# Kernel tuning notes

Hardware: AMD Instinct MI355X
Metric: run time of the kernel (lower is better)

Reference implementation:

```python
import jax, jax.numpy as jnp
import numpy as np

B, S, F_IN = 64, 168, 10
D, H, L = 512, 8, 4
HID, F_OUT, N_FUT = 2048, 1, 48
EPS = 1e-9


def _pos_encoding(d, position=168):
    pos = np.arange(position)[:, None].astype(np.float32)
    i = np.arange(d)[None, :].astype(np.float32)
    angle = pos / np.power(10000.0, 2.0 * (np.floor(i / 2.0)) / np.float32(d))
    angle[:, 0::2] = np.sin(angle[:, 0::2])
    angle[:, 1::2] = np.cos(angle[:, 1::2])
    return jnp.asarray(angle[None, ...], dtype=jnp.float32)  # [1, position, d]


def setup_inputs() -> dict:
    key = jax.random.key(0)
    ks = iter(jax.random.split(key, 64))
    s = 0.02

    def w(shape):
        return (jax.random.normal(next(ks), shape, jnp.float32) * s)

    inp = {
        "x": jax.random.normal(next(ks), (B, S, F_IN), jnp.float32),
        "mask": jnp.triu(jnp.ones((S, S), jnp.float32), k=1)[None, None],  # [1,1,S,S]
        "in_w": w((F_IN, D)), "in_b": jnp.zeros((D,), jnp.float32),
        "wq_w": w((L, D, D * H)), "wq_b": jnp.zeros((L, D * H), jnp.float32),
        "wk_w": w((L, D, D * H)), "wk_b": jnp.zeros((L, D * H), jnp.float32),
        "wv_w": w((L, D, D * H)), "wv_b": jnp.zeros((L, D * H), jnp.float32),
        "dn_w": w((L, D * H, D)), "dn_b": jnp.zeros((L, D), jnp.float32),
        "mh_w": w((L, D, HID)), "mh_b": jnp.zeros((L, HID), jnp.float32),
        "mo_w": w((L, HID, D)), "mo_b": jnp.zeros((L, D), jnp.float32),
        "ln1_g": jnp.ones((L, D), jnp.float32), "ln1_b": jnp.zeros((L, D), jnp.float32),
        "ln3_g": jnp.ones((L, D), jnp.float32), "ln3_b": jnp.zeros((L, D), jnp.float32),
        "out_w": w((D, F_OUT)), "out_b": jnp.zeros((F_OUT,), jnp.float32),
    }
    return inp


def _ln(h, g, b):
    m = jnp.mean(h, axis=-1, keepdims=True)
    v = jnp.mean((h - m) ** 2, axis=-1, keepdims=True)
    return (h - m) * jax.lax.rsqrt(v + EPS) * g + b


def _split(t):  # [B,S,H*D] -> [B,H,S,D]
    return t.reshape(B, S, H, D).transpose(0, 2, 1, 3)


def reference(x, mask, in_w, in_b, wq_w, wq_b, wk_w, wk_b, wv_w, wv_b,
              dn_w, dn_b, mh_w, mh_b, mo_w, mo_b,
              ln1_g, ln1_b, ln3_g, ln3_b, out_w, out_b):
    pe = _pos_encoding(D)  # [1,168,D]
    h = x @ in_w + in_b
    h = h * jnp.sqrt(jnp.float32(D)) + pe[:, :S, :]
    inv_sqrt_d = 1.0 / jnp.sqrt(jnp.float32(D))
    for i in range(L):
        q = _split(h @ wq_w[i] + wq_b[i])
        k = _split(h @ wk_w[i] + wk_b[i])
        v = _split(h @ wv_w[i] + wv_b[i])
        scores = jnp.einsum('bhqd,bhkd->bhqk', q, k) * inv_sqrt_d
        scores = scores + mask * (-1e9)
        attn_w = jax.nn.softmax(scores, axis=-1)
        att = jnp.einsum('bhqk,bhkd->bhqd', attn_w, v)
        att = att.transpose(0, 2, 1, 3).reshape(B, S, H * D)
        att = att @ dn_w[i] + dn_b[i]
        h1 = _ln(att + h, ln1_g[i], ln1_b[i])
        mlp = jax.nn.relu(h1 @ mh_w[i] + mh_b[i]) @ mo_w[i] + mo_b[i]
        h = _ln(mlp + h1, ln3_g[i], ln3_b[i])
    out = h @ out_w + out_b
    return out[:, -N_FUT:, :]
```

## Files before the change

### kernel.cpp

```cpp
#include <hip/hip_runtime.h>
#include <hip/hip_bf16.h>

typedef __bf16 bf16;
typedef __bf16 bf16x8 __attribute__((ext_vector_type(8)));
typedef float f32x4 __attribute__((ext_vector_type(4)));

#define MODE_BIAS 1
#define MODE_RELU 2
#define MODE_BF16 4
#define MODE_F32  8
#define MODE_RES  16
#define MODE_RESB 32
#define MODE_QKV  128

__device__ __forceinline__ void stage16(const bf16* g, bf16* l)
{
  __builtin_amdgcn_global_load_lds(
      (const __attribute__((address_space(1))) void*)g,
      (__attribute__((address_space(3))) void*)l, 16, 0, 0);
}

__global__ __launch_bounds__(256) void gemm2(
    const bf16* __restrict__ A, const bf16* __restrict__ B,
    float* __restrict__ Cf, bf16* __restrict__ Cb,
    const float* __restrict__ bias, const float* __restrict__ resf,
    const bf16* __restrict__ resb,
    int N, int K, int lda, int ldb, int ldc, long qstride, int mode)
{
  __shared__ __attribute__((aligned(16))) bf16 smem[24576];
  bf16* sA = smem;
  bf16* sB = smem + 12288;

  int tid  = threadIdx.x;
  int lane = tid & 63;
  int wave = tid >> 6;
  int wm = (wave >> 1) * 64;
  int wn = (wave & 1) * 64;

  int nwg = gridDim.x * gridDim.y;
  int i0  = blockIdx.y * gridDim.x + blockIdx.x;
  int q   = nwg >> 3, r = nwg & 7;
  int xcd = i0 & 7, jj = i0 >> 3;
  int lid = (xcd < r ? xcd * (q + 1) : r * (q + 1) + (xcd - r) * q) + jj;
  int bx = lid % gridDim.x;
  int by = lid / gridDim.x;
  int bm0 = bx * 128;
  int bn0 = by * 128;

  f32x4 acc[4][4];
  #pragma unroll
  for (int i = 0; i < 4; ++i)
    #pragma unroll
    for (int j = 0; j < 4; ++j)
      #pragma unroll
      for (int rr = 0; rr < 4; ++rr) acc[i][j][rr] = 0.f;

  int seg0 = wave, seg1 = wave + 4;
  int csw = ((lane & 3) ^ ((lane >> 3) & 3)) * 16;
  int r0s = seg0 * 16 + (lane >> 2);
  int r1s = seg1 * 16 + (lane >> 2);
  int rx = ((lane >> 4) ^ ((lane >> 1) & 3)) * 8;

  const char* gA0 = (const char*)A + ((long)(bm0 + r0s) * lda) * 2 + csw;
  const char* gA1 = (const char*)A + ((long)(bm0 + r1s) * lda) * 2 + csw;
  const char* gB0 = (const char*)B + ((long)(bn0 + r0s) * ldb) * 2 + csw;
  const char* gB1 = (const char*)B + ((long)(bn0 + r1s) * ldb) * 2 + csw;

  int nt = K >> 5;

  stage16((const bf16*)gA0, sA + seg0 * 512);
  stage16((const bf16*)gA1, sA + seg1 * 512);
  stage16((const bf16*)gB0, sB + seg0 * 512);
  stage16((const bf16*)gB1, sB + seg1 * 512);
  stage16((const bf16*)(gA0 + 64), sA + 4096 + seg0 * 512);
  stage16((const bf16*)(gA1 + 64), sA + 4096 + seg1 * 512);
  stage16((const bf16*)(gB0 + 64), sB + 4096 + seg0 * 512);
  stage16((const bf16*)(gB1 + 64), sB + 4096 + seg1 * 512);

  int slot = 0, sslot = 2;
  for (int t = 0; t < nt; ++t) {
    if (t + 2 < nt) {
      long ob = (long)(t + 2) * 64;
      int so = sslot * 4096;
      stage16((const bf16*)(gA0 + ob), sA + so + seg0 * 512);
      stage16((const bf16*)(gA1 + ob), sA + so + seg1 * 512);
      stage16((const bf16*)(gB0 + ob), sB + so + seg0 * 512);
      stage16((const bf16*)(gB1 + ob), sB + so + seg1 * 512);
      asm volatile("s_waitcnt vmcnt(8)" ::: "memory");
    } else if (t + 1 < nt) {
      asm volatile("s_waitcnt vmcnt(4)" ::: "memory");
    } else {
      asm volatile("s_waitcnt vmcnt(0)" ::: "memory");
    }
    asm volatile("s_barrier" ::: "memory");
    __builtin_amdgcn_sched_barrier(0);
    int po = slot * 4096;
    bf16x8 aF[4], bF[4];
    #pragma unroll
    for (int i = 0; i < 4; ++i)
      aF[i] = *(const bf16x8*)(&sA[po + (wm + i * 16 + (lane & 15)) * 32 + rx]);
    #pragma unroll
    for (int j = 0; j < 4; ++j)
      bF[j] = *(const bf16x8*)(&sB[po + (wn + j * 16 + (lane & 15)) * 32 + rx]);
    __builtin_amdgcn_s_setprio(1);
    #pragma unroll
    for (int i = 0; i < 4; ++i)
      #pragma unroll
      for (int j = 0; j < 4; ++j)
        acc[i][j] = __builtin_amdgcn_mfma_f32_16x16x32_bf16(aF[i], bF[j], acc[i][j], 0, 0, 0);
    __builtin_amdgcn_s_setprio(0);
    asm volatile("s_waitcnt lgkmcnt(0)" ::: "memory");
    __builtin_amdgcn_sched_barrier(0);
    asm volatile("s_barrier" ::: "memory");
    slot = (slot == 2) ? 0 : slot + 1;
    sslot = (sslot == 2) ? 0 : sslot + 1;
  }

  int lg = lane >> 4;
  int r0 = lg * 4;
  int cc = lane & 15;

  if ((mode & MODE_QKV) && bn0 >= 8192) {
    bf16* sS = smem;
    int nn0 = bn0 - 8192;
    #pragma unroll
    for (int ph = 0; ph < 2; ++ph) {
      if ((wn >> 6) == ph) {
        #pragma unroll
        for (int j = 0; j < 4; ++j) {
          int nl = j * 16 + cc;
          float bv = bias[bn0 + wn + j * 16 + cc];
          #pragma unroll
          for (int i = 0; i < 4; ++i)
            #pragma unroll
            for (int rr = 0; rr < 4; ++rr) {
              int m = wm + i * 16 + r0 + rr;
              sS[nl * 130 + m] = (bf16)(acc[i][j][rr] + bv);
            }
        }
      }
      __syncthreads();
      #pragma unroll
      for (int u = 0; u < 16; ++u) {
        int nrow = u * 4 + wave;
        int d = nn0 + ph * 64 + nrow;
        int hh = d >> 9, dd = d & 511;
        unsigned int pv = *(const unsigned int*)&sS[nrow * 130 + lane * 2];
        int m0 = bm0 + 2 * lane;
        int bl = m0 / 168;
        int s  = m0 - bl * 168;
        *(unsigned int*)&Cb[2 * qstride + ((long)(bl * 8 + hh) * 512 + dd) * 168 + s] = pv;
      }
      __syncthreads();
    }
    return;
  }

  if (mode & (MODE_QKV | MODE_BF16)) {
    bf16* sS = smem;
    #pragma unroll
    for (int j = 0; j < 4; ++j) {
      float bv = (mode & MODE_BIAS) ? bias[bn0 + wn + j * 16 + cc] : 0.f;
      #pragma unroll
      for (int i = 0; i < 4; ++i) {
        #pragma unroll
        for (int rr = 0; rr < 4; ++rr) {
          float v = acc[i][j][rr] + bv;
          if (mode & MODE_RELU) v = fmaxf(v, 0.f);
          sS[(wm + i * 16 + r0 + rr) * 136 + wn + j * 16 + cc] = (bf16)v;
        }
      }
    }
    __syncthreads();
    long base;
    int ldx;
    if (mode & MODE_QKV) {
      int part = bn0 >> 12;
      base = (long)part * qstride + (bn0 & 4095);
      ldx = 4096;
    } else {
      base = (long)bn0;
      ldx = ldc;
    }
    #pragma unroll
    for (int it = 0; it < 8; ++it) {
      int idx = it * 256 + tid;
      int row = idx >> 4, seg = idx & 15;
      bf16x8 v = *(const bf16x8*)&sS[row * 136 + seg * 8];
      *(bf16x8*)&Cb[base + (long)(bm0 + row) * ldx + seg * 8] = v;
    }
    return;
  }

  #pragma unroll
  for (int j = 0; j < 4; ++j) {
    int gn = bn0 + wn + j * 16 + cc;
    float bv = (mode & MODE_BIAS) ? bias[gn] : 0.f;
    #pragma unroll
    for (int i = 0; i < 4; ++i) {
      #pragma unroll
      for (int rr = 0; rr < 4; ++rr) {
        int gm = bm0 + wm + i * 16 + r0 + rr;
        float v = acc[i][j][rr] + bv;
        if (mode & MODE_RES)  v += resf[(long)gm * ldc + gn];
        if (mode & MODE_RESB) v += (float)resb[(long)gm * ldc + gn];
        if (mode & MODE_RELU) v = fmaxf(v, 0.f);
        if (mode & MODE_F32) {
          Cf[(long)gm * ldc + gn] = v;
        } else {
          Cb[(long)gm * ldc + gn] = (bf16)v;
        }
      }
    }
  }
}

__global__ __launch_bounds__(256) void attn_fused(
    const bf16* __restrict__ Q, const bf16* __restrict__ K,
    const bf16* __restrict__ Vt, bf16* __restrict__ O)
{
  __shared__ __attribute__((aligned(16))) bf16 sQ[2 * 64 * 32];
  __shared__ __attribute__((aligned(16))) bf16 sK[2 * 192 * 32];
  __shared__ __attribute__((aligned(16))) bf16 sP[64 * 200];
  __shared__ __attribute__((aligned(16))) bf16 sV[256 * 32];

  int mt = blockIdx.x;
  int bh = blockIdx.y;
  int bl = bh >> 3, h = bh & 7;
  int tid = threadIdx.x, lane = tid & 63, wave = tid >> 6;

  const bf16* Qb = Q + ((long)bl * 168 + mt * 64) * 4096 + h * 512;
  const bf16* Kb = K + (long)bl * 168 * 4096 + h * 512;
  const bf16* Vb = Vt + (long)bh * 512 * 168;

  #pragma unroll
  for (int idx = tid; idx < 64 * 16; idx += 256) {
    int rr = idx >> 4;
    sP[rr * 200 + 176 + (idx & 15)] = (bf16)0.f;
  }

  int srw = wave * 16 + (lane >> 2);
  int scb = ((lane & 3) ^ ((lane >> 3) & 3)) * 16;
  int rx  = ((lane >> 4) ^ ((lane >> 1) & 3)) * 8;

  const char* gQ = (const char*)Qb + (long)srw * 8192 + scb;
  const char* gK = (const char*)Kb + (long)srw * 8192 + scb;

  f32x4 sacc[11];
  #pragma unroll
  for (int j = 0; j < 11; ++j)
    #pragma unroll
    for (int rr = 0; rr < 4; ++rr) sacc[j][rr] = 0.f;

  stage16((const bf16*)gQ, &sQ[wave * 512]);
  stage16((const bf16*)gK, &sK[wave * 512]);
  stage16((const bf16*)(gK + 64 * 8192), &sK[(wave + 4) * 512]);
  stage16((const bf16*)(gK + 128 * 8192), &sK[(wave + 8) * 512]);

  for (int t = 0; t < 16; ++t) {
    int p = t & 1;
    if (t < 15) {
      long ob = (long)(t + 1) * 64;
      int bq = (p ^ 1) * 2048, bk = (p ^ 1) * 6144;
      stage16((const bf16*)(gQ + ob), &sQ[bq + wave * 512]);
      stage16((const bf16*)(gK + ob), &sK[bk + wave * 512]);
      stage16((const bf16*)(gK + 64 * 8192 + ob), &sK[bk + (wave + 4) * 512]);
      stage16((const bf16*)(gK + 128 * 8192 + ob), &sK[bk + (wave + 8) * 512]);
      asm volatile("s_waitcnt vmcnt(4)" ::: "memory");
    } else {
      asm volatile("s_waitcnt vmcnt(0)" ::: "memory");
    }
    asm volatile("s_barrier" ::: "memory");
    __builtin_amdgcn_sched_barrier(0);
    bf16x8 aF = *(const bf16x8*)(&sQ[p * 2048 + (wave * 16 + (lane & 15)) * 32 + rx]);
    __builtin_amdgcn_s_setprio(1);
    #pragma unroll
    for (int j = 0; j < 11; ++j) {
      bf16x8 bF = *(const bf16x8*)(&sK[p * 6144 + (j * 16 + (lane & 15)) * 32 + rx]);
      sacc[j] = __builtin_amdgcn_mfma_f32_16x16x32_bf16(aF, bF, sacc[j], 0, 0, 0);
    }
    __builtin_amdgcn_s_setprio(0);
    asm volatile("s_waitcnt lgkmcnt(0)" ::: "memory");
    __builtin_amdgcn_sched_barrier(0);
    asm volatile("s_barrier" ::: "memory");
  }

  int rbase = wave * 16 + ((lane >> 4) << 2);
  #pragma unroll
  for (int rr = 0; rr < 4; ++rr) {
    int srow = mt * 64 + rbase + rr;
    float mx = -1e30f;
    #pragma unroll
    for (int j = 0; j < 11; ++j) {
      int col = j * 16 + (lane & 15);
      float v = sacc[j][rr] * 0.04419417382415922f;
      v = (col <= srow) ? v : -1e9f;
      sacc[j][rr] = v;
      mx = fmaxf(mx, v);
    }
    #pragma unroll
    for (int off = 1; off < 16; off <<= 1) mx = fmaxf(mx, __shfl_xor(mx, off, 16));
    float sum = 0.f;
    #pragma unroll
    for (int j = 0; j < 11; ++j) {
      float e = __expf(sacc[j][rr] - mx);
      sacc[j][rr] = e;
      sum += e;
    }
    #pragma unroll
    for (int off = 1; off < 16; off <<= 1) sum += __shfl_xor(sum, off, 16);
    float inv = 1.f / sum;
    #pragma unroll
    for (int j = 0; j < 11; ++j)
      sP[(rbase + rr) * 200 + j * 16 + (lane & 15)] = (bf16)(sacc[j][rr] * inv);
  }

  const char* gV = (const char*)Vb + (long)srw * 336 + scb;
  #pragma unroll 1
  for (int nc = 0; nc < 2; ++nc) {
    f32x4 oacc[16];
    #pragma unroll
    for (int t = 0; t < 16; ++t)
      #pragma unroll
      for (int rr = 0; rr < 4; ++rr) oacc[t][rr] = 0.f;

    for (int k0 = 0; k0 < 192; k0 += 32) {
      #pragma unroll
      for (int u = 0; u < 4; ++u)
        stage16((const bf16*)(gV + (long)(nc * 256 + u * 64) * 336 + (long)k0 * 2),
                &sV[(wave + u * 4) * 512]);
      __syncthreads();
      bf16x8 aF = *(const bf16x8*)(&sP[(wave * 16 + (lane & 15)) * 200 + k0 + (lane >> 4) * 8]);
      __builtin_amdgcn_s_setprio(1);
      #pragma unroll
      for (int t = 0; t < 16; ++t) {
        bf16x8 bF = *(const bf16x8*)(&sV[(t * 16 + (lane & 15)) * 32 + rx]);
        oacc[t] = __builtin_amdgcn_mfma_f32_16x16x32_bf16(aF, bF, oacc[t], 0, 0, 0);
      }
      __builtin_amdgcn_s_setprio(0);
      __syncthreads();
    }
    #pragma unroll
    for (int t = 0; t < 16; ++t) {
      int d = nc * 256 + t * 16 + (lane & 15);
      #pragma unroll
      for (int rr = 0; rr < 4; ++rr) {
        int srow = mt * 64 + rbase + rr;
        if (srow < 168)
          O[((long)bl * 168 + srow) * 4096 + h * 512 + d] = (bf16)oacc[t][rr];
      }
    }
  }
}

__global__ __launch_bounds__(256) void transpose_w(const float* __restrict__ in,
                                                   bf16* __restrict__ out,
                                                   int K, int N, long ostride, long obase)
{
  long zi = (long)blockIdx.z * K * N;
  long zo = (long)blockIdx.z * ostride + obase;
  __shared__ float t[32][33];
  int tx = threadIdx.x & 31;
  int ty = threadIdx.x >> 5;
  int n0 = blockIdx.x * 32;
  int k0 = blockIdx.y * 32;
  #pragma unroll
  for (int r = 0; r < 4; ++r) {
    int k = k0 + ty + r * 8, n = n0 + tx;
    if (k < K && n < N) t[ty + r * 8][tx] = in[zi + (long)k * N + n];
  }
  __syncthreads();
  #pragma unroll
  for (int r = 0; r < 4; ++r) {
    int n = n0 + ty + r * 8, k = k0 + tx;
    if (n < N && k < K) out[zo + (long)n * K + k] = (bf16)t[tx][ty + r * 8];
  }
}

__global__ __launch_bounds__(256) void merge_bias(const float* __restrict__ q,
                                                  const float* __restrict__ k,
                                                  const float* __restrict__ v,
                                                  float* __restrict__ o)
{
  int idx = blockIdx.x * 256 + threadIdx.x;
  if (idx >= 4 * 12288) return;
  int l = idx / 12288, r = idx - l * 12288;
  int part = r >> 12, n = r & 4095;
  const float* s = (part == 0) ? q : (part == 1) ? k : v;
  o[idx] = s[l * 4096 + n];
}

__global__ __launch_bounds__(256) void input_proj(const float* __restrict__ x,
                                                  const float* __restrict__ w,
                                                  const float* __restrict__ b,
                                                  float* __restrict__ hf,
                                                  bf16* __restrict__ hb)
{
  long idx = (long)blockIdx.x * 256 + threadIdx.x;
  long row = idx >> 9;
  int d = (int)(idx & 511);
  float acc = b[d];
  const float* xr = x + row * 10;
  #pragma unroll
  for (int f = 0; f < 10; ++f) acc += xr[f] * w[f * 512 + d];
  int s = (int)(row % 168);
  float rate = __expf(-(float)(d & ~1) * (9.210340371976184f / 512.f));
  float ang = (float)s * rate;
  float pe = (d & 1) ? cosf(ang) : sinf(ang);
  float v = acc * 22.627416997969522f + pe;
  hf[idx] = v;
  hb[idx] = (bf16)v;
}

__device__ __forceinline__ float block_sum256(float v, float* red)
{
  #pragma unroll
  for (int o = 32; o > 0; o >>= 1) v += __shfl_xor(v, o, 64);
  if ((threadIdx.x & 63) == 0) red[threadIdx.x >> 6] = v;
  __syncthreads();
  float tot = red[0] + red[1] + red[2] + red[3];
  __syncthreads();
  return tot;
}

__global__ __launch_bounds__(256) void ln_kernel(const float* __restrict__ X,
                                                 const float* __restrict__ g,
                                                 const float* __restrict__ bta,
                                                 float* __restrict__ Yf,
                                                 bf16* __restrict__ Yb)
{
  __shared__ float red[4];
  long row = blockIdx.x;
  int t = threadIdx.x;
  const float* x = X + row * 512;
  float v0 = x[t], v1 = x[t + 256];
  float mean = block_sum256(v0 + v1, red) * (1.f / 512.f);
  float d0 = v0 - mean, d1 = v1 - mean;
  float var = block_sum256(d0 * d0 + d1 * d1, red) * (1.f / 512.f);
  float rs = rsqrtf(var + 1e-9f);
  float y0 = d0 * rs * g[t] + bta[t];
  float y1 = d1 * rs * g[t + 256] + bta[t + 256];
  if (Yf) {
    Yf[row * 512 + t] = y0;
    Yf[row * 512 + t + 256] = y1;
  }
  Yb[row * 512 + t] = (bf16)y0;
  Yb[row * 512 + t + 256] = (bf16)y1;
}

__global__ __launch_bounds__(256) void out_proj(const float* __restrict__ hf,
                                                const float* __restrict__ ow,
                                                const float* __restrict__ ob,
                                                float* __restrict__ out)
{
  int gid = blockIdx.x * 256 + threadIdx.x;
  int wid = gid >> 6;
  int lane = gid & 63;
  if (wid >= 64 * 48) return;
  int b = wid / 48, j = wid - b * 48;
  long row = (long)b * 168 + 120 + j;
  const float* x = hf + row * 512;
  float s = 0.f;
  #pragma unroll
  for (int t = 0; t < 8; ++t) s += x[lane + t * 64] * ow[lane + t * 64];
  #pragma unroll
  for (int o = 32; o > 0; o >>= 1) s += __shfl_xor(s, o, 64);
  if (lane == 0) out[wid] = s + ob[0];
}

extern "C" void kernel_launch(void* const* d_in, const int* in_sizes, int n_in,
                              void* d_out, int out_size, void* d_ws, size_t ws_size,
                              hipStream_t stream)
{
  const float* x     = (const float*)d_in[0];
  const float* in_w  = (const float*)d_in[2];
  const float* in_b  = (const float*)d_in[3];
  const float* wq_w  = (const float*)d_in[4];
  const float* wq_b  = (const float*)d_in[5];
  const float* wk_w  = (const float*)d_in[6];
  const float* wk_b  = (const float*)d_in[7];
  const float* wv_w  = (const float*)d_in[8];
  const float* wv_b  = (const float*)d_in[9];
  const float* dn_w  = (const float*)d_in[10];
  const float* dn_b  = (const float*)d_in[11];
  const float* mh_w  = (const float*)d_in[12];
  const float* mh_b  = (const float*)d_in[13];
  const float* mo_w  = (const float*)d_in[14];
  const float* mo_b  = (const float*)d_in[15];
  const float* ln1_g = (const float*)d_in[16];
  const float* ln1_b = (const float*)d_in[17];
  const float* ln3_g = (const float*)d_in[18];
  const float* ln3_b = (const float*)d_in[19];
  const float* out_w = (const float*)d_in[20];
  const float* out_b = (const float*)d_in[21];
  float* out = (float*)d_out;

  auto al = [](size_t b) { return (b + 255) & ~(size_t)255; };
  size_t off = 0;
  auto alloc = [&](size_t bytes) -> char* {
    char* p = (char*)d_ws + off;
    off += al(bytes);
    return p;
  };

  bf16*  wqkvT = (bf16*)alloc(4L * 12288 * 512 * 2);
  float* qkvB  = (float*)alloc(4L * 12288 * 4);
  bf16*  dnT   = (bf16*)alloc(4L * 512 * 4096 * 2);
  bf16*  mhT   = (bf16*)alloc(4L * 2048 * 512 * 2);
  bf16*  moT   = (bf16*)alloc(4L * 512 * 2048 * 2);
  float* hF    = (float*)alloc(10752L * 512 * 4);
  bf16*  hB    = (bf16*)alloc(10752L * 512 * 2);
  float* Xf    = (float*)alloc(10752L * 512 * 4);

  const int  CB = 16, NC = 4;
  const long Mc = (long)CB * 168;
  const long qstride = Mc * 4096;
  bf16* Qc = (bf16*)alloc((size_t)(3 * qstride) * 2);
  bf16* Kc  = Qc + qstride;
  bf16* Vtc = Qc + 2 * qstride;
  bf16* h1b = Qc;
  bf16* m1c = Qc + 10752L * 512;

  transpose_w<<<dim3(128, 16, 4), 256, 0, stream>>>(wq_w, wqkvT, 512, 4096, 12288L * 512, 0);
  transpose_w<<<dim3(128, 16, 4), 256, 0, stream>>>(wk_w, wqkvT, 512, 4096, 12288L * 512, 4096L * 512);
  transpose_w<<<dim3(128, 16, 4), 256, 0, stream>>>(wv_w, wqkvT, 512, 4096, 12288L * 512, 8192L * 512);
  transpose_w<<<dim3(16, 128, 4), 256, 0, stream>>>(dn_w, dnT, 4096, 512, 512L * 4096, 0);
  transpose_w<<<dim3(64, 16, 4), 256, 0, stream>>>(mh_w, mhT, 512, 2048, 2048L * 512, 0);
  transpose_w<<<dim3(16, 64, 4), 256, 0, stream>>>(mo_w, moT, 2048, 512, 512L * 2048, 0);
  merge_bias<<<(4 * 12288 + 255) / 256, 256, 0, stream>>>(wq_b, wk_b, wv_b, qkvB);

  input_proj<<<10752 * 512 / 256, 256, 0, stream>>>(x, in_w, in_b, hF, hB);

  const int cM = (int)(Mc / 128);

  for (int l = 0; l < 4; ++l) {
    for (int c = 0; c < NC; ++c) {
      long row0 = (long)c * Mc;

      gemm2<<<dim3(cM, 96), 256, 0, stream>>>(
          hB + row0 * 512, wqkvT + (long)l * 12288 * 512, nullptr, Qc,
          qkvB + (long)l * 12288, nullptr, nullptr,
          12288, 512, 512, 512, 0, qstride, MODE_BIAS | MODE_QKV);

      attn_fused<<<dim3(3, CB * 8), 256, 0, stream>>>(Qc, Kc, Vtc, Qc);

      gemm2<<<dim3(cM, 4), 256, 0, stream>>>(
          Qc, dnT + (long)l * 512 * 4096, Xf + row0 * 512, nullptr,
          dn_b + (long)l * 512, hF + row0 * 512, nullptr,
          512, 4096, 4096, 4096, 512, 0, MODE_BIAS | MODE_RES | MODE_F32);
    }

    ln_kernel<<<10752, 256, 0, stream>>>(Xf, ln1_g + l * 512, ln1_b + l * 512,
                                         nullptr, h1b);

    gemm2<<<dim3(84, 16), 256, 0, stream>>>(
        h1b, mhT + (long)l * 2048 * 512, nullptr, m1c,
        mh_b + (long)l * 2048, nullptr, nullptr,
        2048, 512, 512, 512, 2048, 0, MODE_BIAS | MODE_RELU | MODE_BF16);

    gemm2<<<dim3(84, 4), 256, 0, stream>>>(
        m1c, moT + (long)l * 512 * 2048, Xf, nullptr,
        mo_b + (long)l * 512, nullptr, h1b,
        512, 2048, 2048, 2048, 512, 0, MODE_BIAS | MODE_RESB | MODE_F32);

    ln_kernel<<<10752, 256, 0, stream>>>(Xf, ln3_g + l * 512, ln3_b + l * 512,
                                         hF, hB);
  }

  out_proj<<<(64 * 48 * 64) / 256, 256, 0, stream>>>(hF, out_w, out_b, out);
}
```

Before: 3.177 ms.

## Split-K the N=512 GEMMs with atomic fp32 accumulation and shrink LDS staging

The down-projection and MLP-output GEMMs (N=512, K of 4096 or 2048) are split along K over blockIdx.z, into 8 and 4 slices. Each slice atomically adds its partial tile into an fp32 buffer that a new init_acc kernel prefills with bias plus residual. This raises the workgroup count for GEMMs that previously launched only cM×4 or 84×4 blocks, trading that for atomic traffic and an extra pass over the buffer. The GEMM pipeline also drops from triple to double LDS buffering, with a two-phase bf16 epilogue to fit the smaller shared memory, which should help occupancy but exposes more load latency.

```diff
diff --git a/kernel.cpp b/kernel.cpp
--- a/kernel.cpp
+++ b/kernel.cpp
@@ -3,6 +3,7 @@
 
 typedef __bf16 bf16;
 typedef __bf16 bf16x8 __attribute__((ext_vector_type(8)));
+typedef __bf16 bf16x4v __attribute__((ext_vector_type(4)));
 typedef float f32x4 __attribute__((ext_vector_type(4)));
 
 #define MODE_BIAS 1
@@ -12,6 +13,7 @@
 #define MODE_RES  16
 #define MODE_RESB 32
 #define MODE_QKV  128
+#define MODE_ATOMIC 256
 
 __device__ __forceinline__ void stage16(const bf16* g, bf16* l)
 {
@@ -27,9 +29,9 @@
     const bf16* __restrict__ resb,
     int N, int K, int lda, int ldb, int ldc, long qstride, int mode)
 {
-  __shared__ __attribute__((aligned(16))) bf16 smem[24576];
+  __shared__ __attribute__((aligned(16))) bf16 smem[16384];
   bf16* sA = smem;
-  bf16* sB = smem + 12288;
+  bf16* sB = smem + 8192;
 
   int tid  = threadIdx.x;
   int lane = tid & 63;
@@ -46,6 +48,7 @@
   int by = lid / gridDim.x;
   int bm0 = bx * 128;
   int bn0 = by * 128;
+  long ks = (long)blockIdx.z * K;
 
   f32x4 acc[4][4];
   #pragma unroll
@@ -61,10 +64,10 @@
   int r1s = seg1 * 16 + (lane >> 2);
   int rx = ((lane >> 4) ^ ((lane >> 1) & 3)) * 8;
 
-  const char* gA0 = (const char*)A + ((long)(bm0 + r0s) * lda) * 2 + csw;
-  const char* gA1 = (const char*)A + ((long)(bm0 + r1s) * lda) * 2 + csw;
-  const char* gB0 = (const char*)B + ((long)(bn0 + r0s) * ldb) * 2 + csw;
-  const char* gB1 = (const char*)B + ((long)(bn0 + r1s) * ldb) * 2 + csw;
+  const char* gA0 = (const char*)A + ((long)(bm0 + r0s) * lda + ks) * 2 + csw;
+  const char* gA1 = (const char*)A + ((long)(bm0 + r1s) * lda + ks) * 2 + csw;
+  const char* gB0 = (const char*)B + ((long)(bn0 + r0s) * ldb + ks) * 2 + csw;
+  const char* gB1 = (const char*)B + ((long)(bn0 + r1s) * ldb + ks) * 2 + csw;
 
   int nt = K >> 5;
 
@@ -72,29 +75,23 @@
   stage16((const bf16*)gA1, sA + seg1 * 512);
   stage16((const bf16*)gB0, sB + seg0 * 512);
   stage16((const bf16*)gB1, sB + seg1 * 512);
-  stage16((const bf16*)(gA0 + 64), sA + 4096 + seg0 * 512);
-  stage16((const bf16*)(gA1 + 64), sA + 4096 + seg1 * 512);
-  stage16((const bf16*)(gB0 + 64), sB + 4096 + seg0 * 512);
-  stage16((const bf16*)(gB1 + 64), sB + 4096 + seg1 * 512);
-
-  int slot = 0, sslot = 2;
+
   for (int t = 0; t < nt; ++t) {
-    if (t + 2 < nt) {
-      long ob = (long)(t + 2) * 64;
-      int so = sslot * 4096;
+    int p = t & 1;
+    if (t + 1 < nt) {
+      long ob = (long)(t + 1) * 64;
+      int so = (p ^ 1) * 4096;
       stage16((const bf16*)(gA0 + ob), sA + so + seg0 * 512);
       stage16((const bf16*)(gA1 + ob), sA + so + seg1 * 512);
       stage16((const bf16*)(gB0 + ob), sB + so + seg0 * 512);
       stage16((const bf16*)(gB1 + ob), sB + so + seg1 * 512);
-      asm volatile("s_waitcnt vmcnt(8)" ::: "memory");
-    } else if (t + 1 < nt) {
       asm volatile("s_waitcnt vmcnt(4)" ::: "memory");
     } else {
       asm volatile("s_waitcnt vmcnt(0)" ::: "memory");
     }
     asm volatile("s_barrier" ::: "memory");
     __builtin_amdgcn_sched_barrier(0);
-    int po = slot * 4096;
+    int po = p * 4096;
     bf16x8 aF[4], bF[4];
     #pragma unroll
     for (int i = 0; i < 4; ++i)
@@ -112,13 +109,26 @@
     asm volatile("s_waitcnt lgkmcnt(0)" ::: "memory");
     __builtin_amdgcn_sched_barrier(0);
     asm volatile("s_barrier" ::: "memory");
-    slot = (slot == 2) ? 0 : slot + 1;
-    sslot = (sslot == 2) ? 0 : sslot + 1;
   }
 
   int lg = lane >> 4;
   int r0 = lg * 4;
   int cc = lane & 15;
+
+  if (mode & MODE_ATOMIC) {
+    #pragma unroll
+    for (int j = 0; j < 4; ++j) {
+      int gn = bn0 + wn + j * 16 + cc;
+      #pragma unroll
+      for (int i = 0; i < 4; ++i)
+        #pragma unroll
+        for (int rr = 0; rr < 4; ++rr) {
+          int gm = bm0 + wm + i * 16 + r0 + rr;
+          unsafeAtomicAdd(&Cf[(long)gm * ldc + gn], acc[i][j][rr]);
+        }
+    }
+    return;
+  }
 
   if ((mode & MODE_QKV) && bn0 >= 8192) {
     bf16* sS = smem;
@@ -158,20 +168,6 @@
 
   if (mode & (MODE_QKV | MODE_BF16)) {
     bf16* sS = smem;
-    #pragma unroll
-    for (int j = 0; j < 4; ++j) {
-      float bv = (mode & MODE_BIAS) ? bias[bn0 + wn + j * 16 + cc] : 0.f;
-      #pragma unroll
-      for (int i = 0; i < 4; ++i) {
-        #pragma unroll
-        for (int rr = 0; rr < 4; ++rr) {
-          float v = acc[i][j][rr] + bv;
-          if (mode & MODE_RELU) v = fmaxf(v, 0.f);
-          sS[(wm + i * 16 + r0 + rr) * 136 + wn + j * 16 + cc] = (bf16)v;
-        }
-      }
-    }
-    __syncthreads();
     long base;
     int ldx;
     if (mode & MODE_QKV) {
@@ -183,11 +179,31 @@
       ldx = ldc;
     }
     #pragma unroll
-    for (int it = 0; it < 8; ++it) {
-      int idx = it * 256 + tid;
-      int row = idx >> 4, seg = idx & 15;
-      bf16x8 v = *(const bf16x8*)&sS[row * 136 + seg * 8];
-      *(bf16x8*)&Cb[base + (long)(bm0 + row) * ldx + seg * 8] = v;
+    for (int ph = 0; ph < 2; ++ph) {
+      if ((wm >> 6) == ph) {
+        #pragma unroll
+        for (int j = 0; j < 4; ++j) {
+          float bv = (mode & MODE_BIAS) ? bias[bn0 + wn + j * 16 + cc] : 0.f;
+          #pragma unroll
+          for (int i = 0; i < 4; ++i) {
+            #pragma unroll
+            for (int rr = 0; rr < 4; ++rr) {
+              float v = acc[i][j][rr] + bv;
+              if (mode & MODE_RELU) v = fmaxf(v, 0.f);
+              sS[(i * 16 + r0 + rr) * 136 + wn + j * 16 + cc] = (bf16)v;
+            }
+          }
+        }
+      }
+      __syncthreads();
+      #pragma unroll
+      for (int it = 0; it < 4; ++it) {
+        int idx = it * 256 + tid;
+        int row = idx >> 4, seg = idx & 15;
+        bf16x8 v = *(const bf16x8*)&sS[row * 136 + seg * 8];
+        *(bf16x8*)&Cb[base + (long)(bm0 + ph * 64 + row) * ldx + seg * 8] = v;
+      }
+      __syncthreads();
     }
     return;
   }
@@ -213,6 +229,25 @@
       }
     }
   }
+}
+
+__global__ __launch_bounds__(256) void init_acc(
+    float* __restrict__ Xf, const float* __restrict__ srcF,
+    const bf16* __restrict__ srcB, const float* __restrict__ bias, long n)
+{
+  long i = ((long)blockIdx.x * 256 + threadIdx.x) * 4;
+  if (i >= n) return;
+  int d = (int)(i & 511);
+  float4 bv = *(const float4*)&bias[d];
+  float4 v;
+  if (srcF) {
+    v = *(const float4*)&srcF[i];
+  } else {
+    bf16x4v s = *(const bf16x4v*)&srcB[i];
+    v.x = (float)s[0]; v.y = (float)s[1]; v.z = (float)s[2]; v.w = (float)s[3];
+  }
+  v.x += bv.x; v.y += bv.y; v.z += bv.z; v.w += bv.w;
+  *(float4*)&Xf[i] = v;
 }
 
 __global__ __launch_bounds__(256) void attn_fused(
@@ -544,10 +579,12 @@
 
       attn_fused<<<dim3(3, CB * 8), 256, 0, stream>>>(Qc, Kc, Vtc, Qc);
 
-      gemm2<<<dim3(cM, 4), 256, 0, stream>>>(
+      init_acc<<<(int)(Mc * 512 / 1024), 256, 0, stream>>>(
+          Xf + row0 * 512, hF + row0 * 512, nullptr, dn_b + (long)l * 512, Mc * 512);
+      gemm2<<<dim3(cM, 4, 8), 256, 0, stream>>>(
           Qc, dnT + (long)l * 512 * 4096, Xf + row0 * 512, nullptr,
-          dn_b + (long)l * 512, hF + row0 * 512, nullptr,
-          512, 4096, 4096, 4096, 512, 0, MODE_BIAS | MODE_RES | MODE_F32);
+          nullptr, nullptr, nullptr,
+          512, 512, 4096, 4096, 512, 0, MODE_ATOMIC);
     }
 
     ln_kernel<<<10752, 256, 0, stream>>>(Xf, ln1_g + l * 512, ln1_b + l * 512,
@@ -558,10 +595,12 @@
         mh_b + (long)l * 2048, nullptr, nullptr,
         2048, 512, 512, 512, 2048, 0, MODE_BIAS | MODE_RELU | MODE_BF16);
 
-    gemm2<<<dim3(84, 4), 256, 0, stream>>>(
+    init_acc<<<10752 * 512 / 1024, 256, 0, stream>>>(
+        Xf, nullptr, h1b, mo_b + (long)l * 512, 10752L * 512);
+    gemm2<<<dim3(84, 4, 4), 256, 0, stream>>>(
         m1c, moT + (long)l * 512 * 2048, Xf, nullptr,
-        mo_b + (long)l * 512, nullptr, h1b,
-        512, 2048, 2048, 2048, 512, 0, MODE_BIAS | MODE_RESB | MODE_F32);
+        nullptr, nullptr, nullptr,
+        512, 512, 2048, 2048, 512, 0, MODE_ATOMIC);
 
     ln_kernel<<<10752, 256, 0, stream>>>(Xf, ln3_g + l * 512, ln3_b + l * 512,
                                          hF, hB);
```

Result: no change. 3.239 ms (+1.9%).
